# Kernel tuning notes

Hardware: AMD Instinct MI355X
Metric: run time of the kernel (lower is better)

The kernel has to match this reference:

```python
import jax, jax.numpy as jnp
import numpy as np
from jax import lax

# Multi-scale VAR tokenizer encode: per scale, bilinear-resize the residual latent,
# FSQ-quantize it (Cosmos DI16x16 quantizer, levels [8,8,8,5,5,5]), then subtract the
# upsampled ResidualBlock(conv3x3 -> GELU -> conv3x3) reconstruction from the latent.

RESOLUTIONS = [(1, 1), (2, 2), (4, 4), (6, 6), (8, 8), (10, 10), (12, 12), (16, 16)]
LEVELS = np.array([8.0, 8.0, 8.0, 5.0, 5.0, 5.0], dtype=np.float32)  # FSQ levels, 6 channels
C, HIDDEN = 6, 48  # channels, channels * expansion_factor(8)
FSQ_EPS = 1e-3


def _resize(x, hw):
    # matches torch F.interpolate(mode='bilinear', align_corners=False) (half-pixel, no antialias)
    b, c = x.shape[0], x.shape[1]
    return jax.image.resize(x, (b, c, hw[0], hw[1]), method='bilinear', antialias=False)


def _fsq_quantize(z):
    # z: [B, 6, H, W] float32 -> codes in [-1, 1] quantized to per-channel levels
    l = jnp.asarray(LEVELS).reshape(1, C, 1, 1)
    half_l = (l - 1.0) * (1.0 + FSQ_EPS) / 2.0
    offset = jnp.where(jnp.mod(l, 2.0) == 0.0, 0.5, 0.0)
    shift = jnp.arctanh(offset / half_l)
    bounded = jnp.tanh(z + shift) * half_l - offset
    quantized = bounded + lax.stop_gradient(jnp.round(bounded) - bounded)  # straight-through
    half_width = jnp.floor(l / 2.0)
    return quantized / half_width


def _conv3x3(x, w, b):
    y = lax.conv_general_dilated(x, w, window_strides=(1, 1), padding='SAME',
                                 dimension_numbers=('NCHW', 'OIHW', 'NCHW'))
    return y + b.reshape(1, -1, 1, 1)


def _residual_block(x, w1, b1, w2, b2):
    h = _conv3x3(x, w1, b1)
    h = jax.nn.gelu(h, approximate=False)  # nn.GELU default = exact erf
    return _conv3x3(h, w2, b2)


def setup_inputs() -> dict:
    key = jax.random.key(0)
    k0, k1, k2 = jax.random.split(key, 3)
    B = 2048
    n = len(RESOLUTIONS)
    latents = jax.random.normal(k0, (B, C, 16, 16), dtype=jnp.float32)
    w1 = jax.random.normal(k1, (n, HIDDEN, C, 3, 3), dtype=jnp.float32) * 0.05
    b1 = jnp.zeros((n, HIDDEN), dtype=jnp.float32)
    w2 = jax.random.normal(k2, (n, C, HIDDEN, 3, 3), dtype=jnp.float32) * 0.05
    b2 = jnp.zeros((n, C), dtype=jnp.float32)
    return {"latents": latents, "w1": w1, "b1": b1, "w2": w2, "b2": b2}


def reference(latents, w1, b1, w2, b2):
    f = latents
    full_hw = f.shape[-2:]
    tokens = []
    for i, (h, w) in enumerate(RESOLUTIONS):
        f_curr = _resize(f, (h, w))
        r = _fsq_quantize(f_curr)  # tup[1] of Cosmos FSQ quantizer: quantized codes
        tokens.append(r)
        if i < len(RESOLUTIONS) - 1:
            z = _residual_block(r, w1[i], b1[i], w2[i], b2[i])
            z = _resize(z, full_hw)
            f = f - z
    # concatenate per-scale tokens flattened over (C,H,W) -> [B, 6*(1+4+16+36+64+100+144+256)] = [B, 3726]
    return jnp.concatenate([t.reshape(t.shape[0], -1) for t in tokens], axis=-1)
```

## Files before the change

kernel.cpp:

```cpp
#include <hip/hip_runtime.h>
#include <math.h>

#define NTHREADS 256

__constant__ int c_RESA[8] = {1, 2, 4, 6, 8, 10, 12, 16};
__constant__ int c_OFF6[8] = {0, 6, 30, 126, 342, 726, 1326, 2190};

__device__ __forceinline__ void mk_tap(int o, float invs, int insz,
                                       int* i0, int* i1, float* w0, float* w1) {
    float fy = __fsub_rn(__fmul_rn(__fadd_rn((float)o, 0.5f), invs), 0.5f);
    float fl = floorf(fy);
    int y0 = (int)fl;
    float k0 = __fsub_rn(1.0f, fabsf(__fsub_rn(fy, fl)));
    float k1 = __fsub_rn(1.0f, fabsf(__fsub_rn(fy, __fadd_rn(fl, 1.0f))));
    bool v0 = (y0 >= 0);
    bool v1 = (y0 + 1 <= insz - 1);
    k0 = v0 ? k0 : 0.0f;
    k1 = v1 ? k1 : 0.0f;
    float ssum = __fadd_rn(k0, k1);
    *w0 = __fdiv_rn(k0, ssum);
    *w1 = __fdiv_rn(k1, ssum);
    *i0 = v0 ? y0 : 0;
    *i1 = v1 ? (y0 + 1) : (insz - 1);
}

__global__ void __launch_bounds__(NTHREADS)
var_tokenizer_kernel(const float* __restrict__ latents,
                     const float* __restrict__ w1g, const float* __restrict__ b1g,
                     const float* __restrict__ w2g, const float* __restrict__ b2g,
                     float* __restrict__ out) {
    __shared__ float f_l[6 * 256];
    __shared__ float r_pad[6 * 196];
    __shared__ __align__(16) float h_pm[196 * 48];
    __shared__ float z_l[6 * 144];
    __shared__ int   dti0[16]; __shared__ int dti1[16];
    __shared__ float dtw0[16]; __shared__ float dtw1[16];
    __shared__ int   uti0[16]; __shared__ int uti1[16];
    __shared__ float utw0[16]; __shared__ float utw1[16];

    const int item = blockIdx.x;
    const int tid  = threadIdx.x;
    const int wv   = __builtin_amdgcn_readfirstlane(tid >> 6);
    const int lane = tid & 63;

    const float* lat  = latents + (size_t)item * 1536;
    float*       outb = out + (size_t)item * 3726;

    for (int i = tid; i < 1536; i += NTHREADS) f_l[i] = lat[i];
    for (int i = tid; i < 6 * 196;  i += NTHREADS) r_pad[i] = 0.0f;
    for (int i = tid; i < 196 * 48; i += NTHREADS) h_pm[i] = 0.0f;

    const float HL8 = (8.0f - 1.0f) * (1.0f + 1.0e-3f) / 2.0f;
    const float HL5 = (5.0f - 1.0f) * (1.0f + 1.0e-3f) / 2.0f;
    const float SH8 = (float)atanh((double)(0.5f / HL8));

    __syncthreads();

    for (int s = 0; s < 8; ++s) {
        const int R  = c_RESA[s];
        const int HW = R * R;
        const bool last = (s == 7);

        if (tid < R) {
            float invs = __fdiv_rn(1.0f, __fdiv_rn((float)R, 16.0f));
            mk_tap(tid, invs, 16, &dti0[tid], &dti1[tid], &dtw0[tid], &dtw1[tid]);
        } else if (tid >= 64 && tid < 80 && !last) {
            int o = tid - 64;
            float invs = __fdiv_rn(1.0f, __fdiv_rn(16.0f, (float)R));
            mk_tap(o, invs, R, &uti0[o], &uti1[o], &utw0[o], &utw1[o]);
        }
        __syncthreads();

        const int off = c_OFF6[s];
        for (int t = tid; t < 6 * HW; t += NTHREADS) {
            int ox = t % R; int rest = t / R; int oy = rest % R; int c = rest / R;
            int y0 = dti0[oy], y1 = dti1[oy], x0 = dti0[ox], x1 = dti1[ox];
            float wy0 = dtw0[oy], wy1 = dtw1[oy], wx0 = dtw0[ox], wx1 = dtw1[ox];
            const float* fc = f_l + c * 256;
            float a00 = fc[y0 * 16 + x0], a01 = fc[y0 * 16 + x1];
            float a10 = fc[y1 * 16 + x0], a11 = fc[y1 * 16 + x1];
            float t0 = __fadd_rn(__fmul_rn(wy0, a00), __fmul_rn(wy1, a10));
            float t1 = __fadd_rn(__fmul_rn(wy0, a01), __fmul_rn(wy1, a11));
            float v  = __fadd_rn(__fmul_rn(wx0, t0), __fmul_rn(wx1, t1));
            bool is8 = (c < 3);
            float hl   = is8 ? HL8 : HL5;
            float offc = is8 ? 0.5f : 0.0f;
            float sh   = is8 ? SH8 : 0.0f;
            float arg  = __fadd_rn(v, sh);
            float th   = (float)tanh((double)arg);
            float bounded = __fsub_rn(__fmul_rn(th, hl), offc);
            float q = __fmul_rn(rintf(bounded), is8 ? 0.25f : 0.5f);
            outb[off + t] = q;
            if (!last) r_pad[c * 196 + (oy + 1) * 14 + (ox + 1)] = q;
        }
        if (last) break;
        __syncthreads();

        const float* w1s = w1g + (size_t)s * 48 * 54;
        const float* b1s = b1g + (size_t)s * 48;
        for (int pb = 0; pb < HW; pb += 64) {
            int p = pb + lane;
            bool act = p < HW;
            int pc = act ? p : 0;
            int py = pc / R, px = pc - py * R;
            int pbase = py * 14 + px;
            int q = pbase + 15;
            int rot = q & 7;
            float patch[6][9];
            #pragma unroll
            for (int ci = 0; ci < 6; ++ci) {
                const float* rp = r_pad + ci * 196 + pbase;
                #pragma unroll
                for (int dy = 0; dy < 3; ++dy) {
                    patch[ci][dy * 3 + 0] = rp[dy * 14 + 0];
                    patch[ci][dy * 3 + 1] = rp[dy * 14 + 1];
                    patch[ci][dy * 3 + 2] = rp[dy * 14 + 2];
                }
            }
            for (int kk = 0; kk < 12; ++kk) {
                int k = wv * 12 + kk;
                const float* wk = w1s + k * 54;
                float acc = 0.0f;
                #pragma unroll
                for (int ci = 0; ci < 6; ++ci)
                    #pragma unroll
                    for (int j = 0; j < 9; ++j)
                        acc = __fmaf_rn(wk[ci * 9 + j], patch[ci][j], acc);
                acc = __fadd_rn(acc, b1s[k]);
                float g = __fmul_rn(__fmul_rn(0.5f, acc),
                          __fadd_rn(1.0f, erff(__fdiv_rn(acc, 1.41421356f))));
                if (act) {
                    int pk = (k >> 2) + rot; if (pk >= 12) pk -= 12;
                    h_pm[q * 48 + pk * 4 + (k & 3)] = g;
                }
            }
        }
        __syncthreads();

        const float* w2s = w2g + (size_t)s * 6 * 432;
        const float* b2s = b2g + (size_t)s * 6;
        {
            int p = tid;
            if (p < HW) {
                int py = p / R, px = p - py * R;
                float acc[6];
                #pragma unroll
                for (int co = 0; co < 6; ++co) acc[co] = 0.0f;
                for (int dy = 0; dy < 3; ++dy) {
                    for (int dx = 0; dx < 3; ++dx) {
                        int q = (py + dy) * 14 + (px + dx);
                        const float* hp = h_pm + q * 48;
                        int rot = q & 7;
                        const float* wj = w2s + dy * 3 + dx;
                        #pragma unroll 2
                        for (int c4 = 0; c4 < 12; ++c4) {
                            int pb = c4 + rot; if (pb >= 12) pb -= 12;
                            float4 v = *(const float4*)(hp + pb * 4);
                            const float* wc = wj + c4 * 36;
                            #pragma unroll
                            for (int co = 0; co < 6; ++co) {
                                acc[co] = __fmaf_rn(wc[(co * 48 + 0) * 9], v.x, acc[co]);
                                acc[co] = __fmaf_rn(wc[(co * 48 + 1) * 9], v.y, acc[co]);
                                acc[co] = __fmaf_rn(wc[(co * 48 + 2) * 9], v.z, acc[co]);
                                acc[co] = __fmaf_rn(wc[(co * 48 + 3) * 9], v.w, acc[co]);
                            }
                        }
                    }
                }
                #pragma unroll
                for (int co = 0; co < 6; ++co)
                    z_l[co * HW + p] = __fadd_rn(acc[co], b2s[co]);
            }
        }
        __syncthreads();

        for (int t = tid; t < 1536; t += NTHREADS) {
            int x = t & 15; int y = (t >> 4) & 15; int c = t >> 8;
            int y0 = uti0[y], y1 = uti1[y], x0 = uti0[x], x1 = uti1[x];
            float wy0 = utw0[y], wy1 = utw1[y], wx0 = utw0[x], wx1 = utw1[x];
            const float* zc = z_l + c * HW;
            float a00 = zc[y0 * R + x0], a01 = zc[y0 * R + x1];
            float a10 = zc[y1 * R + x0], a11 = zc[y1 * R + x1];
            float t0 = __fadd_rn(__fmul_rn(wy0, a00), __fmul_rn(wy1, a10));
            float t1 = __fadd_rn(__fmul_rn(wy0, a01), __fmul_rn(wy1, a11));
            float zv = __fadd_rn(__fmul_rn(wx0, t0), __fmul_rn(wx1, t1));
            f_l[t] = __fsub_rn(f_l[t], zv);
        }
        __syncthreads();
    }
}

extern "C" void kernel_launch(void* const* d_in, const int* in_sizes, int n_in,
                              void* d_out, int out_size, void* d_ws, size_t ws_size,
                              hipStream_t stream) {
    const float* latents = (const float*)d_in[0];
    const float* w1 = (const float*)d_in[1];
    const float* b1 = (const float*)d_in[2];
    const float* w2 = (const float*)d_in[3];
    const float* b2 = (const float*)d_in[4];
    float* out = (float*)d_out;
    int nitems = in_sizes[0] / 1536;
    var_tokenizer_kernel<<<nitems, NTHREADS, 0, stream>>>(latents, w1, b1, w2, b2, out);
}
```

Before: 947.2 us.

## Chunk hidden channels into three passes to shrink LDS footprint

The 48 hidden channels of the first conv are processed in three chunks of 16, each written to a small 196x20 LDS buffer and immediately consumed by the second conv, with accumulators kept in registers across chunks. This cuts per-block shared memory from about 37 KB to about 15 KB so more blocks can reside per CU. Each wave now computes 4 hidden channels with the patch loaded once per chunk, and the z buffer reuses the same storage. The cost is extra barriers, re-reading the input patch three times, and re-zeroing the pad border each scale.

After: 3.114 ms. +228.8%, slower.

```diff
diff --git a/kernel.cpp b/kernel.cpp
--- a/kernel.cpp
+++ b/kernel.cpp
@@ -2,6 +2,7 @@
 #include <math.h>
 
 #define NTHREADS 256
+#define HSTRIDE 20
 
 __constant__ int c_RESA[8] = {1, 2, 4, 6, 8, 10, 12, 16};
 __constant__ int c_OFF6[8] = {0, 6, 30, 126, 342, 726, 1326, 2190};
@@ -29,10 +30,9 @@
                      const float* __restrict__ w1g, const float* __restrict__ b1g,
                      const float* __restrict__ w2g, const float* __restrict__ b2g,
                      float* __restrict__ out) {
-    __shared__ float f_l[6 * 256];
+    __shared__ float f_l[1536];
     __shared__ float r_pad[6 * 196];
-    __shared__ __align__(16) float h_pm[196 * 48];
-    __shared__ float z_l[6 * 144];
+    __shared__ __align__(16) float h16[196 * HSTRIDE];
     __shared__ int   dti0[16]; __shared__ int dti1[16];
     __shared__ float dtw0[16]; __shared__ float dtw1[16];
     __shared__ int   uti0[16]; __shared__ int uti1[16];
@@ -47,8 +47,8 @@
     float*       outb = out + (size_t)item * 3726;
 
     for (int i = tid; i < 1536; i += NTHREADS) f_l[i] = lat[i];
-    for (int i = tid; i < 6 * 196;  i += NTHREADS) r_pad[i] = 0.0f;
-    for (int i = tid; i < 196 * 48; i += NTHREADS) h_pm[i] = 0.0f;
+    for (int i = tid; i < 6 * 196;        i += NTHREADS) r_pad[i] = 0.0f;
+    for (int i = tid; i < 196 * HSTRIDE;  i += NTHREADS) h16[i] = 0.0f;
 
     const float HL8 = (8.0f - 1.0f) * (1.0f + 1.0e-3f) / 2.0f;
     const float HL5 = (5.0f - 1.0f) * (1.0f + 1.0e-3f) / 2.0f;
@@ -68,6 +68,20 @@
             int o = tid - 64;
             float invs = __fdiv_rn(1.0f, __fdiv_rn(16.0f, (float)R));
             mk_tap(o, invs, R, &uti0[o], &uti1[o], &utw0[o], &utw1[o]);
+        }
+        if (!last) {
+            int nb = 4 * R + 4;
+            for (int t = tid; t < nb; t += NTHREADS) {
+                int wy, wx;
+                if (t < R + 2)          { wy = 0;     wx = t; }
+                else if (t < 2 * R + 4) { wy = R + 1; wx = t - (R + 2); }
+                else { int u = t - (2 * R + 4); wy = 1 + (u >> 1); wx = (u & 1) ? (R + 1) : 0; }
+                float* hp = h16 + (wy * 14 + wx) * HSTRIDE;
+                float4 z4 = make_float4(0.f, 0.f, 0.f, 0.f);
+                *(float4*)(hp +  0) = z4; *(float4*)(hp +  4) = z4;
+                *(float4*)(hp +  8) = z4; *(float4*)(hp + 12) = z4;
+                *(float4*)(hp + 16) = z4;
+            }
         }
         __syncthreads();
 
@@ -96,80 +110,103 @@
         if (last) break;
         __syncthreads();
 
-        const float* w1s = w1g + (size_t)s * 48 * 54;
+        const float* w1s = w1g + (size_t)s * 2592;
         const float* b1s = b1g + (size_t)s * 48;
-        for (int pb = 0; pb < HW; pb += 64) {
-            int p = pb + lane;
-            bool act = p < HW;
-            int pc = act ? p : 0;
-            int py = pc / R, px = pc - py * R;
-            int pbase = py * 14 + px;
-            int q = pbase + 15;
-            int rot = q & 7;
-            float patch[6][9];
-            #pragma unroll
-            for (int ci = 0; ci < 6; ++ci) {
-                const float* rp = r_pad + ci * 196 + pbase;
-                #pragma unroll
-                for (int dy = 0; dy < 3; ++dy) {
-                    patch[ci][dy * 3 + 0] = rp[dy * 14 + 0];
-                    patch[ci][dy * 3 + 1] = rp[dy * 14 + 1];
-                    patch[ci][dy * 3 + 2] = rp[dy * 14 + 2];
+        const float* w2s = w2g + (size_t)s * 2592;
+        const float* b2s = b2g + (size_t)s * 6;
+        float ac0 = 0.f, ac1 = 0.f, ac2 = 0.f, ac3 = 0.f, ac4 = 0.f, ac5 = 0.f;
+
+        for (int hh = 0; hh < 3; ++hh) {
+            {
+                int kbase = hh * 16 + wv * 4;
+                const float* wk0 = w1s + (kbase + 0) * 54;
+                const float* wk1 = w1s + (kbase + 1) * 54;
+                const float* wk2 = w1s + (kbase + 2) * 54;
+                const float* wk3 = w1s + (kbase + 3) * 54;
+                for (int pb = 0; pb < HW; pb += 64) {
+                    int p = pb + lane;
+                    bool act = p < HW;
+                    int pc = act ? p : 0;
+                    int py = pc / R, px = pc - py * R;
+                    int pbase = py * 14 + px;
+                    float patch[54];
+                    #pragma unroll
+                    for (int ci = 0; ci < 6; ++ci) {
+                        const float* rp = r_pad + ci * 196 + pbase;
+                        #pragma unroll
+                        for (int dy = 0; dy < 3; ++dy) {
+                            patch[ci * 9 + dy * 3 + 0] = rp[dy * 14 + 0];
+                            patch[ci * 9 + dy * 3 + 1] = rp[dy * 14 + 1];
+                            patch[ci * 9 + dy * 3 + 2] = rp[dy * 14 + 2];
+                        }
+                    }
+                    float a0 = 0.f, a1 = 0.f, a2 = 0.f, a3 = 0.f;
+                    #pragma unroll
+                    for (int w = 0; w < 54; ++w) {
+                        float pv = patch[w];
+                        a0 = __fmaf_rn(wk0[w], pv, a0);
+                        a1 = __fmaf_rn(wk1[w], pv, a1);
+                        a2 = __fmaf_rn(wk2[w], pv, a2);
+                        a3 = __fmaf_rn(wk3[w], pv, a3);
+                    }
+                    a0 = __fadd_rn(a0, b1s[kbase + 0]);
+                    a1 = __fadd_rn(a1, b1s[kbase + 1]);
+                    a2 = __fadd_rn(a2, b1s[kbase + 2]);
+                    a3 = __fadd_rn(a3, b1s[kbase + 3]);
+                    float4 hv;
+                    hv.x = __fmul_rn(__fmul_rn(0.5f, a0),
+                           __fadd_rn(1.0f, erff(__fdiv_rn(a0, 1.41421356f))));
+                    hv.y = __fmul_rn(__fmul_rn(0.5f, a1),
+                           __fadd_rn(1.0f, erff(__fdiv_rn(a1, 1.41421356f))));
+                    hv.z = __fmul_rn(__fmul_rn(0.5f, a2),
+                           __fadd_rn(1.0f, erff(__fdiv_rn(a2, 1.41421356f))));
+                    hv.w = __fmul_rn(__fmul_rn(0.5f, a3),
+                           __fadd_rn(1.0f, erff(__fdiv_rn(a3, 1.41421356f))));
+                    if (act)
+                        *(float4*)&h16[(pbase + 15) * HSTRIDE + wv * 4] = hv;
                 }
             }
-            for (int kk = 0; kk < 12; ++kk) {
-                int k = wv * 12 + kk;
-                const float* wk = w1s + k * 54;
-                float acc = 0.0f;
-                #pragma unroll
-                for (int ci = 0; ci < 6; ++ci)
-                    #pragma unroll
-                    for (int j = 0; j < 9; ++j)
-                        acc = __fmaf_rn(wk[ci * 9 + j], patch[ci][j], acc);
-                acc = __fadd_rn(acc, b1s[k]);
-                float g = __fmul_rn(__fmul_rn(0.5f, acc),
-                          __fadd_rn(1.0f, erff(__fdiv_rn(acc, 1.41421356f))));
-                if (act) {
-                    int pk = (k >> 2) + rot; if (pk >= 12) pk -= 12;
-                    h_pm[q * 48 + pk * 4 + (k & 3)] = g;
+            __syncthreads();
+
+            {
+                int p = tid;
+                if (p < HW) {
+                    int py = p / R, px = p - py * R;
+                    #pragma unroll
+                    for (int dy = 0; dy < 3; ++dy)
+                    #pragma unroll
+                    for (int dx = 0; dx < 3; ++dx) {
+                        int qq = (py + dy) * 14 + (px + dx);
+                        const float* hb = h16 + qq * HSTRIDE;
+                        const float* wj = w2s + dy * 3 + dx;
+                        #pragma unroll
+                        for (int c4 = 0; c4 < 4; ++c4) {
+                            float4 v = *(const float4*)(hb + c4 * 4);
+                            int ch = hh * 16 + c4 * 4;
+#define S3ACC(AC, CO) \
+    AC = __fmaf_rn(wj[(CO * 48 + ch + 0) * 9], v.x, AC); \
+    AC = __fmaf_rn(wj[(CO * 48 + ch + 1) * 9], v.y, AC); \
+    AC = __fmaf_rn(wj[(CO * 48 + ch + 2) * 9], v.z, AC); \
+    AC = __fmaf_rn(wj[(CO * 48 + ch + 3) * 9], v.w, AC);
+                            S3ACC(ac0, 0) S3ACC(ac1, 1) S3ACC(ac2, 2)
+                            S3ACC(ac3, 3) S3ACC(ac4, 4) S3ACC(ac5, 5)
+#undef S3ACC
+                        }
+                    }
                 }
             }
-        }
-        __syncthreads();
-
-        const float* w2s = w2g + (size_t)s * 6 * 432;
-        const float* b2s = b2g + (size_t)s * 6;
+            __syncthreads();
+        }
+
         {
             int p = tid;
             if (p < HW) {
-                int py = p / R, px = p - py * R;
-                float acc[6];
-                #pragma unroll
-                for (int co = 0; co < 6; ++co) acc[co] = 0.0f;
-                for (int dy = 0; dy < 3; ++dy) {
-                    for (int dx = 0; dx < 3; ++dx) {
-                        int q = (py + dy) * 14 + (px + dx);
-                        const float* hp = h_pm + q * 48;
-                        int rot = q & 7;
-                        const float* wj = w2s + dy * 3 + dx;
-                        #pragma unroll 2
-                        for (int c4 = 0; c4 < 12; ++c4) {
-                            int pb = c4 + rot; if (pb >= 12) pb -= 12;
-                            float4 v = *(const float4*)(hp + pb * 4);
-                            const float* wc = wj + c4 * 36;
-                            #pragma unroll
-                            for (int co = 0; co < 6; ++co) {
-                                acc[co] = __fmaf_rn(wc[(co * 48 + 0) * 9], v.x, acc[co]);
-                                acc[co] = __fmaf_rn(wc[(co * 48 + 1) * 9], v.y, acc[co]);
-                                acc[co] = __fmaf_rn(wc[(co * 48 + 2) * 9], v.z, acc[co]);
-                                acc[co] = __fmaf_rn(wc[(co * 48 + 3) * 9], v.w, acc[co]);
-                            }
-                        }
-                    }
-                }
-                #pragma unroll
-                for (int co = 0; co < 6; ++co)
-                    z_l[co * HW + p] = __fadd_rn(acc[co], b2s[co]);
+                h16[0 * HW + p] = __fadd_rn(ac0, b2s[0]);
+                h16[1 * HW + p] = __fadd_rn(ac1, b2s[1]);
+                h16[2 * HW + p] = __fadd_rn(ac2, b2s[2]);
+                h16[3 * HW + p] = __fadd_rn(ac3, b2s[3]);
+                h16[4 * HW + p] = __fadd_rn(ac4, b2s[4]);
+                h16[5 * HW + p] = __fadd_rn(ac5, b2s[5]);
             }
         }
         __syncthreads();
@@ -178,7 +215,7 @@
             int x = t & 15; int y = (t >> 4) & 15; int c = t >> 8;
             int y0 = uti0[y], y1 = uti1[y], x0 = uti0[x], x1 = uti1[x];
             float wy0 = utw0[y], wy1 = utw1[y], wx0 = utw0[x], wx1 = utw1[x];
-            const float* zc = z_l + c * HW;
+            const float* zc = h16 + c * HW;
             float a00 = zc[y0 * R + x0], a01 = zc[y0 * R + x1];
             float a10 = zc[y1 * R + x0], a11 = zc[y1 * R + x1];
             float t0 = __fadd_rn(__fmul_rn(wy0, a00), __fmul_rn(wy1, a10));
```

## Use channel-group-major hidden layout, 4-output conv1 blocking, and magic-number division

Applied to the files above, without the earlier changes.

The hidden activation buffer moves from a pixel-major layout with a rotated channel index to a channel-group-major float4 layout, so conv1 writes and conv2 reads are contiguous 16-byte accesses without the rotation arithmetic. Conv1 now computes four hidden channels per pass, reusing each patch value across four FMAs and storing a float4. Integer divisions by the resolution are replaced with multiply-shift magic constants, and the GELU divide becomes a multiply by 1/sqrt(2). The new layout changes the LDS bank-conflict pattern, four accumulators raise register pressure, and multiplying by 1/sqrt(2) instead of dividing can shift erf inputs by rounding.

Result: faster. 817.0 us (-13.7%).

```diff
diff --git a/kernel.cpp b/kernel.cpp
--- a/kernel.cpp
+++ b/kernel.cpp
@@ -5,6 +5,8 @@
 
 __constant__ int c_RESA[8] = {1, 2, 4, 6, 8, 10, 12, 16};
 __constant__ int c_OFF6[8] = {0, 6, 30, 126, 342, 726, 1326, 2190};
+__constant__ unsigned c_MAGIC[8] = {1048576u, 524288u, 262144u, 174763u,
+                                    131072u, 104858u, 87382u, 65536u};
 
 __device__ __forceinline__ void mk_tap(int o, float invs, int insz,
                                        int* i0, int* i1, float* w0, float* w1) {
@@ -24,14 +26,19 @@
     *i1 = v1 ? (y0 + 1) : (insz - 1);
 }
 
+__device__ __forceinline__ float gelu_exact(float x) {
+    return __fmul_rn(__fmul_rn(0.5f, x),
+                     __fadd_rn(1.0f, erff(__fmul_rn(x, 0.70710678118654752440f))));
+}
+
 __global__ void __launch_bounds__(NTHREADS)
 var_tokenizer_kernel(const float* __restrict__ latents,
                      const float* __restrict__ w1g, const float* __restrict__ b1g,
                      const float* __restrict__ w2g, const float* __restrict__ b2g,
                      float* __restrict__ out) {
-    __shared__ float f_l[6 * 256];
+    __shared__ float f_l[1536];
     __shared__ float r_pad[6 * 196];
-    __shared__ __align__(16) float h_pm[196 * 48];
+    __shared__ __align__(16) float h4[12 * 196 * 4];
     __shared__ float z_l[6 * 144];
     __shared__ int   dti0[16]; __shared__ int dti1[16];
     __shared__ float dtw0[16]; __shared__ float dtw1[16];
@@ -47,8 +54,8 @@
     float*       outb = out + (size_t)item * 3726;
 
     for (int i = tid; i < 1536; i += NTHREADS) f_l[i] = lat[i];
-    for (int i = tid; i < 6 * 196;  i += NTHREADS) r_pad[i] = 0.0f;
-    for (int i = tid; i < 196 * 48; i += NTHREADS) h_pm[i] = 0.0f;
+    for (int i = tid; i < 6 * 196;      i += NTHREADS) r_pad[i] = 0.0f;
+    for (int i = tid; i < 12 * 196 * 4; i += NTHREADS) h4[i] = 0.0f;
 
     const float HL8 = (8.0f - 1.0f) * (1.0f + 1.0e-3f) / 2.0f;
     const float HL5 = (5.0f - 1.0f) * (1.0f + 1.0e-3f) / 2.0f;
@@ -59,6 +66,7 @@
     for (int s = 0; s < 8; ++s) {
         const int R  = c_RESA[s];
         const int HW = R * R;
+        const unsigned M = c_MAGIC[s];
         const bool last = (s == 7);
 
         if (tid < R) {
@@ -73,7 +81,10 @@
 
         const int off = c_OFF6[s];
         for (int t = tid; t < 6 * HW; t += NTHREADS) {
-            int ox = t % R; int rest = t / R; int oy = rest % R; int c = rest / R;
+            int rest = (int)(((unsigned)t * M) >> 20);
+            int ox   = t - rest * R;
+            int c    = (int)(((unsigned)rest * M) >> 20);
+            int oy   = rest - c * R;
             int y0 = dti0[oy], y1 = dti1[oy], x0 = dti0[ox], x1 = dti1[ox];
             float wy0 = dtw0[oy], wy1 = dtw1[oy], wx0 = dtw0[ox], wx1 = dtw1[ox];
             const float* fc = f_l + c * 256;
@@ -96,16 +107,16 @@
         if (last) break;
         __syncthreads();
 
-        const float* w1s = w1g + (size_t)s * 48 * 54;
+        const float* w1s = w1g + (size_t)s * 2592;
         const float* b1s = b1g + (size_t)s * 48;
         for (int pb = 0; pb < HW; pb += 64) {
             int p = pb + lane;
             bool act = p < HW;
             int pc = act ? p : 0;
-            int py = pc / R, px = pc - py * R;
+            int py = (int)(((unsigned)pc * M) >> 20);
+            int px = pc - py * R;
             int pbase = py * 14 + px;
             int q = pbase + 15;
-            int rot = q & 7;
             float patch[6][9];
             #pragma unroll
             for (int ci = 0; ci < 6; ++ci) {
@@ -117,45 +128,54 @@
                     patch[ci][dy * 3 + 2] = rp[dy * 14 + 2];
                 }
             }
-            for (int kk = 0; kk < 12; ++kk) {
-                int k = wv * 12 + kk;
-                const float* wk = w1s + k * 54;
-                float acc = 0.0f;
+            for (int g = 0; g < 3; ++g) {
+                int kb = wv * 12 + g * 4;
+                const float* wk0 = w1s + (kb + 0) * 54;
+                const float* wk1 = w1s + (kb + 1) * 54;
+                const float* wk2 = w1s + (kb + 2) * 54;
+                const float* wk3 = w1s + (kb + 3) * 54;
+                float a0 = 0.f, a1 = 0.f, a2 = 0.f, a3 = 0.f;
                 #pragma unroll
                 for (int ci = 0; ci < 6; ++ci)
                     #pragma unroll
-                    for (int j = 0; j < 9; ++j)
-                        acc = __fmaf_rn(wk[ci * 9 + j], patch[ci][j], acc);
-                acc = __fadd_rn(acc, b1s[k]);
-                float g = __fmul_rn(__fmul_rn(0.5f, acc),
-                          __fadd_rn(1.0f, erff(__fdiv_rn(acc, 1.41421356f))));
+                    for (int j = 0; j < 9; ++j) {
+                        float pv = patch[ci][j];
+                        int wi = ci * 9 + j;
+                        a0 = __fmaf_rn(wk0[wi], pv, a0);
+                        a1 = __fmaf_rn(wk1[wi], pv, a1);
+                        a2 = __fmaf_rn(wk2[wi], pv, a2);
+                        a3 = __fmaf_rn(wk3[wi], pv, a3);
+                    }
+                float4 hv;
+                hv.x = gelu_exact(__fadd_rn(a0, b1s[kb + 0]));
+                hv.y = gelu_exact(__fadd_rn(a1, b1s[kb + 1]));
+                hv.z = gelu_exact(__fadd_rn(a2, b1s[kb + 2]));
+                hv.w = gelu_exact(__fadd_rn(a3, b1s[kb + 3]));
                 if (act) {
-                    int pk = (k >> 2) + rot; if (pk >= 12) pk -= 12;
-                    h_pm[q * 48 + pk * 4 + (k & 3)] = g;
+                    int c4u = wv * 3 + g;
+                    *(float4*)&h4[(c4u * 196 + q) * 4] = hv;
                 }
             }
         }
         __syncthreads();
 
-        const float* w2s = w2g + (size_t)s * 6 * 432;
+        const float* w2s = w2g + (size_t)s * 2592;
         const float* b2s = b2g + (size_t)s * 6;
         {
             int p = tid;
             if (p < HW) {
-                int py = p / R, px = p - py * R;
+                int py = (int)(((unsigned)p * M) >> 20);
+                int px = p - py * R;
                 float acc[6];
                 #pragma unroll
                 for (int co = 0; co < 6; ++co) acc[co] = 0.0f;
                 for (int dy = 0; dy < 3; ++dy) {
                     for (int dx = 0; dx < 3; ++dx) {
-                        int q = (py + dy) * 14 + (px + dx);
-                        const float* hp = h_pm + q * 48;
-                        int rot = q & 7;
+                        int qq = (py + dy) * 14 + (px + dx);
                         const float* wj = w2s + dy * 3 + dx;
                         #pragma unroll 2
                         for (int c4 = 0; c4 < 12; ++c4) {
-                            int pb = c4 + rot; if (pb >= 12) pb -= 12;
-                            float4 v = *(const float4*)(hp + pb * 4);
+                            float4 v = *(const float4*)&h4[(c4 * 196 + qq) * 4];
                             const float* wc = wj + c4 * 36;
                             #pragma unroll
                             for (int co = 0; co < 6; ++co) {
```
